# Optimization experiments

Hardware: AMD Instinct MI355X
Metric: run time of the kernel (lower is better)

The kernel has to match this reference:

```python
import jax, jax.numpy as jnp
import numpy as np

B, S, HID = 1, 2048, 2048
NH, NKV, D = 32, 8, 64
GROUPS = NH // NKV
THETA = 10000.0


def _rope_tables(seq_len, dim):
    inv_freq = 1.0 / (THETA ** (jnp.arange(0, dim, 2, dtype=jnp.float32) / dim))
    t = jnp.arange(seq_len, dtype=jnp.float32)
    freqs = jnp.outer(t, inv_freq)            # [S, D/2]
    emb = jnp.concatenate([freqs, freqs], axis=-1)  # [S, D]
    return jnp.cos(emb), jnp.sin(emb)


def _rotate_half(x):
    x1, x2 = jnp.split(x, 2, axis=-1)
    return jnp.concatenate([-x2, x1], axis=-1)


def setup_inputs() -> dict:
    key = jax.random.key(0)
    ks = jax.random.split(key, 8)
    hidden_states = jax.random.normal(ks[0], (B, S, HID), dtype=jnp.float32)
    # additive causal mask, 0 on/below diagonal, -1e9 above
    causal = jnp.tril(jnp.ones((S, S), dtype=bool))
    attention_mask = jnp.where(causal, 0.0, -1e9).astype(jnp.float32)[None, None]
    sc = 0.02
    Wq = sc * jax.random.normal(ks[1], (NH * D, HID), dtype=jnp.float32)
    bq = jnp.zeros((NH * D,), dtype=jnp.float32)
    Wk = sc * jax.random.normal(ks[2], (NKV * D, HID), dtype=jnp.float32)
    bk = jnp.zeros((NKV * D,), dtype=jnp.float32)
    Wv = sc * jax.random.normal(ks[3], (NKV * D, HID), dtype=jnp.float32)
    bv = jnp.zeros((NKV * D,), dtype=jnp.float32)
    Wo = sc * jax.random.normal(ks[4], (HID, NH * D), dtype=jnp.float32)
    return {"hidden_states": hidden_states, "attention_mask": attention_mask,
            "Wq": Wq, "bq": bq, "Wk": Wk, "bk": bk, "Wv": Wv, "bv": bv, "Wo": Wo}


def reference(hidden_states, attention_mask, Wq, bq, Wk, bk, Wv, bv, Wo):
    b, s, _ = hidden_states.shape
    q = (hidden_states @ Wq.T + bq).reshape(b, s, NH, D).transpose(0, 2, 1, 3)   # [B,NH,S,D]
    k = (hidden_states @ Wk.T + bk).reshape(b, s, NKV, D).transpose(0, 2, 1, 3)  # [B,NKV,S,D]
    v = (hidden_states @ Wv.T + bv).reshape(b, s, NKV, D).transpose(0, 2, 1, 3)
    cos, sin = _rope_tables(s, D)
    cos = cos[None, None]; sin = sin[None, None]
    q = q * cos + _rotate_half(q) * sin
    k = k * cos + _rotate_half(k) * sin
    # GQA: repeat KV heads to match query heads
    k = jnp.repeat(k, GROUPS, axis=1)  # [B,NH,S,D]
    v = jnp.repeat(v, GROUPS, axis=1)
    scores = jnp.einsum('bhqd,bhkd->bhqk', q, k) / jnp.sqrt(jnp.float32(D))
    scores = jnp.clip(scores, -50.0, 50.0)
    scores = scores + attention_mask
    probs = jax.nn.softmax(scores.astype(jnp.float32), axis=-1).astype(q.dtype)
    attn = jnp.einsum('bhqk,bhkd->bhqd', probs, v)
    attn = attn.transpose(0, 2, 1, 3).reshape(b, s, NH * D)
    return attn @ Wo.T
```

## Files before the change

kernel.cpp:

```cpp
#include <hip/hip_runtime.h>
#include <hip/hip_bf16.h>
#include <stdint.h>

typedef unsigned short u16;
typedef unsigned int u32;

#define S_LEN 2048
#define HID 2048
#define NH 32
#define NKV 8
#define HD 64
#define PIT 2080

using f32x4 = __attribute__((ext_vector_type(4))) float;
using bfrag = __attribute__((ext_vector_type(8))) short;

__device__ __forceinline__ float b2f(u16 u) {
  union { u32 i; float f; } c; c.i = ((u32)u) << 16; return c.f;
}
__device__ __forceinline__ u16 f2b(float f) {
  union { float f; u32 i; } c; c.f = f;
  u32 r = c.i + 0x7fffu + ((c.i >> 16) & 1u);
  return (u16)(r >> 16);
}
__device__ __forceinline__ uint4 cvt8(const float* __restrict__ p) {
  float4 a = *(const float4*)p;
  float4 b = *(const float4*)(p + 4);
  uint4 r;
  r.x = (u32)f2b(a.x) | ((u32)f2b(a.y) << 16);
  r.y = (u32)f2b(a.z) | ((u32)f2b(a.w) << 16);
  r.z = (u32)f2b(b.x) | ((u32)f2b(b.y) << 16);
  r.w = (u32)f2b(b.z) | ((u32)f2b(b.w) << 16);
  return r;
}

__device__ __forceinline__ void gl2lds16(const u16* g, u16* l) {
  __builtin_amdgcn_global_load_lds(
      (const __attribute__((address_space(1))) void*)g,
      (__attribute__((address_space(3))) void*)l,
      16, 0, 0);
}

#define WAITBAR(N) asm volatile("s_waitcnt vmcnt(" #N ")\ns_barrier" ::: "memory")

__global__ void conv_all(const float* __restrict__ hid, const float* __restrict__ Wq,
                         const float* __restrict__ Wk, const float* __restrict__ Wv,
                         u16* __restrict__ hidb, u16* __restrict__ Wqkvb) {
  int row = blockIdx.x;
  int col = threadIdx.x * 8;
  const float* src; u16* dst;
  if (row < 2048)      { src = hid + (size_t)row * 2048;          dst = hidb  + (size_t)row * PIT; }
  else if (row < 4096) { src = Wq + (size_t)(row - 2048) * 2048;  dst = Wqkvb + (size_t)(row - 2048) * PIT; }
  else if (row < 4608) { src = Wk + (size_t)(row - 4096) * 2048;  dst = Wqkvb + (size_t)(row - 4096 + 2048) * PIT; }
  else                 { src = Wv + (size_t)(row - 4608) * 2048;  dst = Wqkvb + (size_t)(row - 4608 + 2560) * PIT; }
  *(uint4*)(dst + col) = cvt8(src + col);
}

__global__ void conv_f2b_p(const float* __restrict__ in, u16* __restrict__ out, int n8) {
  int i = blockIdx.x * 256 + threadIdx.x;
  if (i >= n8) return;
  int row = i >> 8;
  int col = (i & 255) * 8;
  *(uint4*)(out + (size_t)row * PIT + col) = cvt8(in + (size_t)row * 2048 + col);
}

__global__ __launch_bounds__(256, 3) void gemm_qkv(
    const u16* __restrict__ A, const u16* __restrict__ B,
    const float* __restrict__ bq, const float* __restrict__ bk, const float* __restrict__ bv,
    u16* __restrict__ Qb, u16* __restrict__ Kb, u16* __restrict__ Vt)
{
  __shared__ __align__(16) u16 As[3 * 2048];
  __shared__ __align__(16) u16 Bs[3 * 4096];
  __shared__ __align__(16) u16 strip_s[4][16 * 72];

  const int tid  = threadIdx.x;
  const int m0   = blockIdx.y * 64;
  const int n0   = blockIdx.x * 128;
  const int lane = tid & 63;
  const int w    = tid >> 6;
  const int wm   = w >> 1, wn = w & 1;
  const int quad = lane >> 4, l16 = lane & 15;

  const int srow = tid >> 2;
  const int scol = (tid & 3) * 8;
  const u16* ga = A + (size_t)(m0 + srow) * PIT + scol;
  const u16* gb = B + (size_t)(n0 + srow) * PIT + scol;

#define STAGE_G(bi, k0)                                                         \
  do {                                                                          \
    gl2lds16(ga + (k0), As + (bi) * 2048 + tid * 8);                            \
    gl2lds16(gb + (k0), Bs + (bi) * 4096 + tid * 8);                            \
    gl2lds16(gb + (size_t)64 * PIT + (k0), Bs + (bi) * 4096 + 2048 + tid * 8);  \
  } while (0)

  f32x4 zero = {0.f, 0.f, 0.f, 0.f};
  f32x4 acc[2][4];
#pragma unroll
  for (int mi = 0; mi < 2; ++mi)
#pragma unroll
    for (int ni = 0; ni < 4; ++ni) acc[mi][ni] = zero;

  STAGE_G(0, 0);
  STAGE_G(1, 32);

  int cur = 0;
  for (int k = 0; k < 64; ++k) {
    if (k < 63) WAITBAR(3);
    else        WAITBAR(0);
    if (k + 2 < 64) {
      int nb = cur + 2; if (nb >= 3) nb -= 3;
      STAGE_G(nb, (k + 2) * 32);
    }
    const u16* as = As + cur * 2048;
    const u16* bs = Bs + cur * 4096;

    bfrag af[2], bf[4];
#pragma unroll
    for (int i = 0; i < 2; ++i)
      af[i] = *(const bfrag*)&as[(wm * 32 + i * 16 + l16) * 32 + quad * 8];
#pragma unroll
    for (int i = 0; i < 4; ++i)
      bf[i] = *(const bfrag*)&bs[(wn * 64 + i * 16 + l16) * 32 + quad * 8];
#pragma unroll
    for (int mi = 0; mi < 2; ++mi)
#pragma unroll
      for (int ni = 0; ni < 4; ++ni)
        acc[mi][ni] = __builtin_amdgcn_mfma_f32_16x16x32_bf16(af[mi], bf[ni], acc[mi][ni], 0, 0, 0);

    cur += 1; if (cur == 3) cur = 0;
  }
#undef STAGE_G

  u16* strip = strip_s[w];
  const int rr = lane >> 2;
  const int co = (lane & 3) * 8;

  if (n0 < 2048) {
#pragma unroll
    for (int mi = 0; mi < 2; ++mi) {
#pragma unroll
      for (int n01 = 0; n01 < 2; ++n01)
#pragma unroll
        for (int i = 0; i < 4; ++i) {
          int d  = n01 * 16 + l16;
          int c1 = n0 + wn * 64 + d;
          float x1 = acc[mi][n01][i]     + bq[c1];
          float x2 = acc[mi][n01 + 2][i] + bq[c1 + 32];
          float inv = exp2f(-(float)d * 0.41524101186092034f);
          float ang = (float)(m0 + wm * 32 + mi * 16 + quad * 4 + i) * inv;
          float cs = cosf(ang), sn = sinf(ang);
          strip[(quad * 4 + i) * 72 + d]      = f2b(x1 * cs - x2 * sn);
          strip[(quad * 4 + i) * 72 + d + 32] = f2b(x2 * cs + x1 * sn);
        }
      uint4 v0 = *(const uint4*)&strip[rr * 72 + co];
      uint4 v1 = *(const uint4*)&strip[rr * 72 + 32 + co];
      size_t gb2 = (size_t)(m0 + wm * 32 + mi * 16 + rr) * 2048 + n0 + wn * 64;
      *(uint4*)(Qb + gb2 + co)      = v0;
      *(uint4*)(Qb + gb2 + 32 + co) = v1;
    }
  } else if (n0 < 2560) {
    int cb = (n0 - 2048) + wn * 64;
#pragma unroll
    for (int mi = 0; mi < 2; ++mi) {
#pragma unroll
      for (int n01 = 0; n01 < 2; ++n01)
#pragma unroll
        for (int i = 0; i < 4; ++i) {
          int d  = n01 * 16 + l16;
          int cg = cb + d;
          float x1 = acc[mi][n01][i]     + bk[cg];
          float x2 = acc[mi][n01 + 2][i] + bk[cg + 32];
          float inv = exp2f(-(float)d * 0.41524101186092034f);
          float ang = (float)(m0 + wm * 32 + mi * 16 + quad * 4 + i) * inv;
          float cs = cosf(ang), sn = sinf(ang);
          strip[(quad * 4 + i) * 72 + d]      = f2b(x1 * cs - x2 * sn);
          strip[(quad * 4 + i) * 72 + d + 32] = f2b(x2 * cs + x1 * sn);
        }
      uint4 v0 = *(const uint4*)&strip[rr * 72 + co];
      uint4 v1 = *(const uint4*)&strip[rr * 72 + 32 + co];
      size_t gb2 = (size_t)(m0 + wm * 32 + mi * 16 + rr) * 512 + cb;
      *(uint4*)(Kb + gb2 + co)      = v0;
      *(uint4*)(Kb + gb2 + 32 + co) = v1;
    }
  } else {
    int cgb = (n0 - 2560) + wn * 64;
#pragma unroll
    for (int ni = 0; ni < 4; ++ni) {
      float bvv = bv[cgb + ni * 16 + l16];
#pragma unroll
      for (int mi = 0; mi < 2; ++mi)
#pragma unroll
        for (int i = 0; i < 4; ++i)
          strip[l16 * 72 + mi * 16 + quad * 4 + i] = f2b(acc[mi][ni][i] + bvv);
      uint4 v0 = *(const uint4*)&strip[rr * 72 + co];
      size_t gb2 = (size_t)(cgb + ni * 16 + rr) * PIT + m0 + wm * 32;
      *(uint4*)(Vt + gb2 + co) = v0;
    }
  }
}

__global__ __launch_bounds__(256, 3) void gemm_o(
    const u16* __restrict__ A, const u16* __restrict__ B, float* __restrict__ C)
{
  __shared__ __align__(16) u16 As[3 * 2048];
  __shared__ __align__(16) u16 Bs[3 * 4096];

  const int tid  = threadIdx.x;
  const int m0   = blockIdx.y * 64;
  const int n0   = blockIdx.x * 128;
  const int lane = tid & 63;
  const int w    = tid >> 6;
  const int wm   = w >> 1, wn = w & 1;
  const int quad = lane >> 4, l16 = lane & 15;

  const int srow = tid >> 2;
  const int scol = (tid & 3) * 8;
  const u16* ga = A + (size_t)(m0 + srow) * PIT + scol;
  const u16* gb = B + (size_t)(n0 + srow) * PIT + scol;

#define STAGE_G(bi, k0)                                                         \
  do {                                                                          \
    gl2lds16(ga + (k0), As + (bi) * 2048 + tid * 8);                            \
    gl2lds16(gb + (k0), Bs + (bi) * 4096 + tid * 8);                            \
    gl2lds16(gb + (size_t)64 * PIT + (k0), Bs + (bi) * 4096 + 2048 + tid * 8);  \
  } while (0)

  f32x4 zero = {0.f, 0.f, 0.f, 0.f};
  f32x4 acc[2][4];
#pragma unroll
  for (int mi = 0; mi < 2; ++mi)
#pragma unroll
    for (int ni = 0; ni < 4; ++ni) acc[mi][ni] = zero;

  STAGE_G(0, 0);
  STAGE_G(1, 32);

  int cur = 0;
  for (int k = 0; k < 64; ++k) {
    if (k < 63) WAITBAR(3);
    else        WAITBAR(0);
    if (k + 2 < 64) {
      int nb = cur + 2; if (nb >= 3) nb -= 3;
      STAGE_G(nb, (k + 2) * 32);
    }
    const u16* as = As + cur * 2048;
    const u16* bs = Bs + cur * 4096;

    bfrag af[2], bf[4];
#pragma unroll
    for (int i = 0; i < 2; ++i)
      af[i] = *(const bfrag*)&as[(wm * 32 + i * 16 + l16) * 32 + quad * 8];
#pragma unroll
    for (int i = 0; i < 4; ++i)
      bf[i] = *(const bfrag*)&bs[(wn * 64 + i * 16 + l16) * 32 + quad * 8];
#pragma unroll
    for (int mi = 0; mi < 2; ++mi)
#pragma unroll
      for (int ni = 0; ni < 4; ++ni)
        acc[mi][ni] = __builtin_amdgcn_mfma_f32_16x16x32_bf16(af[mi], bf[ni], acc[mi][ni], 0, 0, 0);

    cur += 1; if (cur == 3) cur = 0;
  }
#undef STAGE_G

#pragma unroll
  for (int ni = 0; ni < 4; ++ni) {
    int col = n0 + wn * 64 + ni * 16 + l16;
#pragma unroll
    for (int mi = 0; mi < 2; ++mi)
#pragma unroll
      for (int i = 0; i < 4; ++i) {
        int row = m0 + wm * 32 + mi * 16 + quad * 4 + i;
        C[(size_t)row * 2048 + col] = acc[mi][ni][i];
      }
  }
}

#define SM_SC 0.18033688011112042f
#define SM_UB 72.134752044448169f

__global__ __launch_bounds__(256, 2) void attn_flash6(
    const u16* __restrict__ Qb, const u16* __restrict__ Kb,
    const u16* __restrict__ Vt, u16* __restrict__ Ab)
{
  __shared__ __align__(16) u16 Ks[3][64 * 64];
  __shared__ __align__(16) u16 Vs[3][64 * 64];
  __shared__ __align__(16) u16 Ps[4][16][72];

  const int h    = blockIdx.x;
  const int p    = blockIdx.y;
  const int kvh  = h >> 2;
  const int tid  = threadIdx.x;
  const int lane = tid & 63;
  const int w    = tid >> 6;
  const int quad = lane >> 4, l16 = lane & 15;

  const int qtA = 31 - p, qtB = p;
  const int nA  = qtA + 1;

  const int c0  = w * 128 + lane;
  const int r0  = c0 >> 3,        s0 = c0 & 7;
  const int r1  = (c0 + 64) >> 3, s1 = (c0 + 64) & 7;
  const int sg0 = s0 ^ (r0 & 7);
  const int sg1 = s1 ^ (r1 & 7);
  const u16* Ksrc0 = Kb + (size_t)r0 * 512 + kvh * 64 + sg0 * 8;
  const u16* Ksrc1 = Kb + (size_t)r1 * 512 + kvh * 64 + sg1 * 8;
  const u16* Vsrc0 = Vt + (size_t)(kvh * 64 + r0) * PIT + sg0 * 8;
  const u16* Vsrc1 = Vt + (size_t)(kvh * 64 + r1) * PIT + sg1 * 8;

#define STAGEKV(buf, kb)                                                        \
  do {                                                                          \
    gl2lds16(Ksrc0 + (size_t)(kb) * 32768, &Ks[buf][0] + c0 * 8);               \
    gl2lds16(Ksrc1 + (size_t)(kb) * 32768, &Ks[buf][0] + (c0 + 64) * 8);        \
    gl2lds16(Vsrc0 + (kb) * 64,            &Vs[buf][0] + c0 * 8);               \
    gl2lds16(Vsrc1 + (kb) * 64,            &Vs[buf][0] + (c0 + 64) * 8);        \
  } while (0)

  STAGEKV(0, 0);
  STAGEKV(1, 1);

  bfrag qfA0, qfA1, qfB0, qfB1;
  {
    const u16* qa = Qb + (size_t)(qtA * 64 + w * 16 + l16) * 2048 + h * 64 + quad * 8;
    const u16* qb = Qb + (size_t)(qtB * 64 + w * 16 + l16) * 2048 + h * 64 + quad * 8;
    qfA0 = *(const bfrag*)qa;  qfA1 = *(const bfrag*)(qa + 32);
    qfB0 = *(const bfrag*)qb;  qfB1 = *(const bfrag*)(qb + 32);
  }
  bfrag q0 = qfA0, q1 = qfA1;

  f32x4 zero = {0.f, 0.f, 0.f, 0.f};
  f32x4 o_acc[4];
  float lpart[4];
#pragma unroll
  for (int nb = 0; nb < 4; ++nb) { o_acc[nb] = zero; lpart[nb] = 0.f; }

  const int swz = (l16 & 7) * 8;
  int qt = qtA;
  int cur = 0;

  for (int t = 0; t < 33; ++t) {
    if (t < 32) WAITBAR(4);
    else        WAITBAR(0);
    if (t + 2 < 33) {
      int kb2 = (t + 2 < nA) ? (t + 2) : (t + 2 - nA);
      int b3 = cur + 2; if (b3 >= 3) b3 -= 3;
      STAGEKV(b3, kb2);
    }
    if (t == nA) { q0 = qfB0; q1 = qfB1; qt = qtB; }

    const u16* ks = &Ks[cur][0];
    const u16* vs = &Vs[cur][0];

    bfrag kf0[4], kf1[4];
#pragma unroll
    for (int nb = 0; nb < 4; ++nb) {
      int row = (nb * 16 + l16) * 64;
      kf0[nb] = *(const bfrag*)&ks[row + ((quad * 8) ^ swz)];
      kf1[nb] = *(const bfrag*)&ks[row + ((32 + quad * 8) ^ swz)];
    }

    const bool diag = (t == nA - 1) || (t == 32);

    f32x4 s_acc[4];
#pragma unroll
    for (int nb = 0; nb < 4; ++nb) {
      s_acc[nb] = __builtin_amdgcn_mfma_f32_16x16x32_bf16(q0, kf0[nb], zero, 0, 0, 0);
      s_acc[nb] = __builtin_amdgcn_mfma_f32_16x16x32_bf16(q1, kf1[nb], s_acc[nb], 0, 0, 0);
    }
    if (diag) {
#pragma unroll
      for (int nb = 0; nb < 4; ++nb)
#pragma unroll
        for (int i = 0; i < 4; ++i) {
          float u = s_acc[nb][i] * SM_SC;
          u = fminf(SM_UB, fmaxf(-SM_UB, u));
          bool msk = (nb * 16 + l16 > w * 16 + quad * 4 + i);
          float pr = msk ? 0.0f : __builtin_amdgcn_exp2f(u);
          lpart[i] += pr;
          Ps[w][quad * 4 + i][nb * 16 + l16] = f2b(pr);
        }
    } else {
#pragma unroll
      for (int nb = 0; nb < 4; ++nb)
#pragma unroll
        for (int i = 0; i < 4; ++i) {
          float u = s_acc[nb][i] * SM_SC;
          u = fminf(SM_UB, fmaxf(-SM_UB, u));
          float pr = __builtin_amdgcn_exp2f(u);
          lpart[i] += pr;
          Ps[w][quad * 4 + i][nb * 16 + l16] = f2b(pr);
        }
    }

    bfrag vf0[4], vf1[4];
#pragma unroll
    for (int nb = 0; nb < 4; ++nb) {
      int row = (nb * 16 + l16) * 64;
      vf0[nb] = *(const bfrag*)&vs[row + ((quad * 8) ^ swz)];
      vf1[nb] = *(const bfrag*)&vs[row + ((32 + quad * 8) ^ swz)];
    }
    {
      bfrag pf0 = *(const bfrag*)&Ps[w][l16][quad * 8];
      bfrag pf1 = *(const bfrag*)&Ps[w][l16][32 + quad * 8];
#pragma unroll
      for (int nb = 0; nb < 4; ++nb) {
        o_acc[nb] = __builtin_amdgcn_mfma_f32_16x16x32_bf16(pf0, vf0[nb], o_acc[nb], 0, 0, 0);
        o_acc[nb] = __builtin_amdgcn_mfma_f32_16x16x32_bf16(pf1, vf1[nb], o_acc[nb], 0, 0, 0);
      }
    }

    if (diag) {
#pragma unroll
      for (int off = 1; off < 16; off <<= 1)
#pragma unroll
        for (int i = 0; i < 4; ++i)
          lpart[i] += __shfl_xor(lpart[i], off, 64);
#pragma unroll
      for (int i = 0; i < 4; ++i) {
        float inv = 1.0f / lpart[i];
        size_t rbase = (size_t)(qt * 64 + w * 16 + quad * 4 + i) * PIT + h * 64;
#pragma unroll
        for (int nb = 0; nb < 4; ++nb)
          Ab[rbase + nb * 16 + l16] = f2b(o_acc[nb][i] * inv);
      }
#pragma unroll
      for (int nb = 0; nb < 4; ++nb) { o_acc[nb] = zero; lpart[nb] = 0.f; }
    }

    cur += 1; if (cur == 3) cur = 0;
  }
}

extern "C" void kernel_launch(void* const* d_in, const int* in_sizes, int n_in,
                              void* d_out, int out_size, void* d_ws, size_t ws_size,
                              hipStream_t stream) {
  const float* hid = (const float*)d_in[0];
  const float* Wq = (const float*)d_in[2];
  const float* bq = (const float*)d_in[3];
  const float* Wk = (const float*)d_in[4];
  const float* bk = (const float*)d_in[5];
  const float* Wv = (const float*)d_in[6];
  const float* bv = (const float*)d_in[7];
  const float* Wo = (const float*)d_in[8];

  u16* hidb  = (u16*)d_ws;
  u16* Wqkvb = hidb + (size_t)2048 * PIT;
  u16* Qb    = Wqkvb + (size_t)3072 * PIT;
  u16* Kb    = Qb + 4194304;
  u16* Vt    = Kb + 1048576;
  u16* Wob   = hidb;
  u16* Ab    = Wqkvb;
  float* Ob  = (float*)d_out;

  conv_all<<<5120, 256, 0, stream>>>(hid, Wq, Wk, Wv, hidb, Wqkvb);

  gemm_qkv<<<dim3(24, 32), 256, 0, stream>>>(hidb, Wqkvb, bq, bk, bv, Qb, Kb, Vt);

  conv_f2b_p<<<2048, 256, 0, stream>>>(Wo, Wob, 524288);

  attn_flash6<<<dim3(32, 16), 256, 0, stream>>>(Qb, Kb, Vt, Ab);

  gemm_o<<<dim3(16, 32), 256, 0, stream>>>(Ab, Wob, Ob);
}
```

Measured before the change: 250.0 us.

## Enlarge GEMM block tiles to 128x128 with 64x64 per-wave subtiles

Both the QKV and output-projection GEMMs move from 64x128 to 128x128 block tiles, so each wave computes a 64x64 subtile with 16 MFMA accumulators instead of 8. This raises MFMA work per LDS fragment load and halves the number of blocks, cutting global and LDS traffic per FLOP. In exchange it uses more registers and LDS, lowers the occupancy bound from 3 to 2 blocks per CU, and leaves fewer blocks (384 and 256) to fill the CUs. The epilogues, the V-transpose store and the wait counts are updated to match.

Result: slower. 273.4 us (+9.3%).

```diff
diff --git a/kernel.cpp b/kernel.cpp
--- a/kernel.cpp
+++ b/kernel.cpp
@@ -64,39 +64,38 @@
   *(uint4*)(out + (size_t)row * PIT + col) = cvt8(in + (size_t)row * 2048 + col);
 }
 
-__global__ __launch_bounds__(256, 3) void gemm_qkv(
+__global__ __launch_bounds__(256, 2) void gemm_qkv(
     const u16* __restrict__ A, const u16* __restrict__ B,
     const float* __restrict__ bq, const float* __restrict__ bk, const float* __restrict__ bv,
     u16* __restrict__ Qb, u16* __restrict__ Kb, u16* __restrict__ Vt)
 {
-  __shared__ __align__(16) u16 As[3 * 2048];
+  __shared__ __align__(16) u16 As[3 * 4096];
   __shared__ __align__(16) u16 Bs[3 * 4096];
   __shared__ __align__(16) u16 strip_s[4][16 * 72];
 
   const int tid  = threadIdx.x;
-  const int m0   = blockIdx.y * 64;
+  const int m0   = blockIdx.y * 128;
   const int n0   = blockIdx.x * 128;
   const int lane = tid & 63;
   const int w    = tid >> 6;
   const int wm   = w >> 1, wn = w & 1;
   const int quad = lane >> 4, l16 = lane & 15;
 
-  const int srow = tid >> 2;
-  const int scol = (tid & 3) * 8;
-  const u16* ga = A + (size_t)(m0 + srow) * PIT + scol;
-  const u16* gb = B + (size_t)(n0 + srow) * PIT + scol;
+  const u16* gA = A + (size_t)(m0 + (tid >> 2)) * PIT + (tid & 3) * 8;
+  const u16* gB = B + (size_t)(n0 + (tid >> 2)) * PIT + (tid & 3) * 8;
 
 #define STAGE_G(bi, k0)                                                         \
   do {                                                                          \
-    gl2lds16(ga + (k0), As + (bi) * 2048 + tid * 8);                            \
-    gl2lds16(gb + (k0), Bs + (bi) * 4096 + tid * 8);                            \
-    gl2lds16(gb + (size_t)64 * PIT + (k0), Bs + (bi) * 4096 + 2048 + tid * 8);  \
+    gl2lds16(gA + (k0), As + (bi) * 4096 + tid * 8);                            \
+    gl2lds16(gA + (size_t)64 * PIT + (k0), As + (bi) * 4096 + 2048 + tid * 8);  \
+    gl2lds16(gB + (k0), Bs + (bi) * 4096 + tid * 8);                            \
+    gl2lds16(gB + (size_t)64 * PIT + (k0), Bs + (bi) * 4096 + 2048 + tid * 8);  \
   } while (0)
 
   f32x4 zero = {0.f, 0.f, 0.f, 0.f};
-  f32x4 acc[2][4];
-#pragma unroll
-  for (int mi = 0; mi < 2; ++mi)
+  f32x4 acc[4][4];
+#pragma unroll
+  for (int mi = 0; mi < 4; ++mi)
 #pragma unroll
     for (int ni = 0; ni < 4; ++ni) acc[mi][ni] = zero;
 
@@ -105,24 +104,24 @@
 
   int cur = 0;
   for (int k = 0; k < 64; ++k) {
-    if (k < 63) WAITBAR(3);
+    if (k < 63) WAITBAR(4);
     else        WAITBAR(0);
     if (k + 2 < 64) {
       int nb = cur + 2; if (nb >= 3) nb -= 3;
       STAGE_G(nb, (k + 2) * 32);
     }
-    const u16* as = As + cur * 2048;
-    const u16* bs = Bs + cur * 4096;
-
-    bfrag af[2], bf[4];
-#pragma unroll
-    for (int i = 0; i < 2; ++i)
-      af[i] = *(const bfrag*)&as[(wm * 32 + i * 16 + l16) * 32 + quad * 8];
+    const u16* as = As + cur * 4096 + wm * 2048;
+    const u16* bs = Bs + cur * 4096 + wn * 2048;
+
+    bfrag af[4], bf[4];
 #pragma unroll
     for (int i = 0; i < 4; ++i)
-      bf[i] = *(const bfrag*)&bs[(wn * 64 + i * 16 + l16) * 32 + quad * 8];
-#pragma unroll
-    for (int mi = 0; mi < 2; ++mi)
+      af[i] = *(const bfrag*)&as[(i * 16 + l16) * 32 + quad * 8];
+#pragma unroll
+    for (int i = 0; i < 4; ++i)
+      bf[i] = *(const bfrag*)&bs[(i * 16 + l16) * 32 + quad * 8];
+#pragma unroll
+    for (int mi = 0; mi < 4; ++mi)
 #pragma unroll
       for (int ni = 0; ni < 4; ++ni)
         acc[mi][ni] = __builtin_amdgcn_mfma_f32_16x16x32_bf16(af[mi], bf[ni], acc[mi][ni], 0, 0, 0);
@@ -132,36 +131,38 @@
 #undef STAGE_G
 
   u16* strip = strip_s[w];
-  const int rr = lane >> 2;
-  const int co = (lane & 3) * 8;
+  const int rr   = lane >> 2;
+  const int co   = (lane & 3) * 8;
+  const int mrow = m0 + wm * 64;
 
   if (n0 < 2048) {
-#pragma unroll
-    for (int mi = 0; mi < 2; ++mi) {
+    int cb = n0 + wn * 64;
+#pragma unroll
+    for (int mi = 0; mi < 4; ++mi) {
 #pragma unroll
       for (int n01 = 0; n01 < 2; ++n01)
 #pragma unroll
         for (int i = 0; i < 4; ++i) {
           int d  = n01 * 16 + l16;
-          int c1 = n0 + wn * 64 + d;
+          int c1 = cb + d;
           float x1 = acc[mi][n01][i]     + bq[c1];
           float x2 = acc[mi][n01 + 2][i] + bq[c1 + 32];
           float inv = exp2f(-(float)d * 0.41524101186092034f);
-          float ang = (float)(m0 + wm * 32 + mi * 16 + quad * 4 + i) * inv;
+          float ang = (float)(mrow + mi * 16 + quad * 4 + i) * inv;
           float cs = cosf(ang), sn = sinf(ang);
           strip[(quad * 4 + i) * 72 + d]      = f2b(x1 * cs - x2 * sn);
           strip[(quad * 4 + i) * 72 + d + 32] = f2b(x2 * cs + x1 * sn);
         }
       uint4 v0 = *(const uint4*)&strip[rr * 72 + co];
       uint4 v1 = *(const uint4*)&strip[rr * 72 + 32 + co];
-      size_t gb2 = (size_t)(m0 + wm * 32 + mi * 16 + rr) * 2048 + n0 + wn * 64;
+      size_t gb2 = (size_t)(mrow + mi * 16 + rr) * 2048 + cb;
       *(uint4*)(Qb + gb2 + co)      = v0;
       *(uint4*)(Qb + gb2 + 32 + co) = v1;
     }
   } else if (n0 < 2560) {
     int cb = (n0 - 2048) + wn * 64;
 #pragma unroll
-    for (int mi = 0; mi < 2; ++mi) {
+    for (int mi = 0; mi < 4; ++mi) {
 #pragma unroll
       for (int n01 = 0; n01 < 2; ++n01)
 #pragma unroll
@@ -171,14 +172,14 @@
           float x1 = acc[mi][n01][i]     + bk[cg];
           float x2 = acc[mi][n01 + 2][i] + bk[cg + 32];
           float inv = exp2f(-(float)d * 0.41524101186092034f);
-          float ang = (float)(m0 + wm * 32 + mi * 16 + quad * 4 + i) * inv;
+          float ang = (float)(mrow + mi * 16 + quad * 4 + i) * inv;
           float cs = cosf(ang), sn = sinf(ang);
           strip[(quad * 4 + i) * 72 + d]      = f2b(x1 * cs - x2 * sn);
           strip[(quad * 4 + i) * 72 + d + 32] = f2b(x2 * cs + x1 * sn);
         }
       uint4 v0 = *(const uint4*)&strip[rr * 72 + co];
       uint4 v1 = *(const uint4*)&strip[rr * 72 + 32 + co];
-      size_t gb2 = (size_t)(m0 + wm * 32 + mi * 16 + rr) * 512 + cb;
+      size_t gb2 = (size_t)(mrow + mi * 16 + rr) * 512 + cb;
       *(uint4*)(Kb + gb2 + co)      = v0;
       *(uint4*)(Kb + gb2 + 32 + co) = v1;
     }
@@ -188,47 +189,48 @@
     for (int ni = 0; ni < 4; ++ni) {
       float bvv = bv[cgb + ni * 16 + l16];
 #pragma unroll
-      for (int mi = 0; mi < 2; ++mi)
+      for (int mi = 0; mi < 4; ++mi)
 #pragma unroll
         for (int i = 0; i < 4; ++i)
           strip[l16 * 72 + mi * 16 + quad * 4 + i] = f2b(acc[mi][ni][i] + bvv);
       uint4 v0 = *(const uint4*)&strip[rr * 72 + co];
-      size_t gb2 = (size_t)(cgb + ni * 16 + rr) * PIT + m0 + wm * 32;
-      *(uint4*)(Vt + gb2 + co) = v0;
-    }
-  }
-}
-
-__global__ __launch_bounds__(256, 3) void gemm_o(
+      uint4 v1 = *(const uint4*)&strip[rr * 72 + 32 + co];
+      size_t gb2 = (size_t)(cgb + ni * 16 + rr) * PIT + mrow;
+      *(uint4*)(Vt + gb2 + co)      = v0;
+      *(uint4*)(Vt + gb2 + 32 + co) = v1;
+    }
+  }
+}
+
+__global__ __launch_bounds__(256, 2) void gemm_o(
     const u16* __restrict__ A, const u16* __restrict__ B, float* __restrict__ C)
 {
-  __shared__ __align__(16) u16 As[3 * 2048];
+  __shared__ __align__(16) u16 As[3 * 4096];
   __shared__ __align__(16) u16 Bs[3 * 4096];
 
   const int tid  = threadIdx.x;
-  const int m0   = blockIdx.y * 64;
+  const int m0   = blockIdx.y * 128;
   const int n0   = blockIdx.x * 128;
   const int lane = tid & 63;
   const int w    = tid >> 6;
   const int wm   = w >> 1, wn = w & 1;
   const int quad = lane >> 4, l16 = lane & 15;
 
-  const int srow = tid >> 2;
-  const int scol = (tid & 3) * 8;
-  const u16* ga = A + (size_t)(m0 + srow) * PIT + scol;
-  const u16* gb = B + (size_t)(n0 + srow) * PIT + scol;
+  const u16* gA = A + (size_t)(m0 + (tid >> 2)) * PIT + (tid & 3) * 8;
+  const u16* gB = B + (size_t)(n0 + (tid >> 2)) * PIT + (tid & 3) * 8;
 
 #define STAGE_G(bi, k0)                                                         \
   do {                                                                          \
-    gl2lds16(ga + (k0), As + (bi) * 2048 + tid * 8);                            \
-    gl2lds16(gb + (k0), Bs + (bi) * 4096 + tid * 8);                            \
-    gl2lds16(gb + (size_t)64 * PIT + (k0), Bs + (bi) * 4096 + 2048 + tid * 8);  \
+    gl2lds16(gA + (k0), As + (bi) * 4096 + tid * 8);                            \
+    gl2lds16(gA + (size_t)64 * PIT + (k0), As + (bi) * 4096 + 2048 + tid * 8);  \
+    gl2lds16(gB + (k0), Bs + (bi) * 4096 + tid * 8);                            \
+    gl2lds16(gB + (size_t)64 * PIT + (k0), Bs + (bi) * 4096 + 2048 + tid * 8);  \
   } while (0)
 
   f32x4 zero = {0.f, 0.f, 0.f, 0.f};
-  f32x4 acc[2][4];
-#pragma unroll
-  for (int mi = 0; mi < 2; ++mi)
+  f32x4 acc[4][4];
+#pragma unroll
+  for (int mi = 0; mi < 4; ++mi)
 #pragma unroll
     for (int ni = 0; ni < 4; ++ni) acc[mi][ni] = zero;
 
@@ -237,24 +239,24 @@
 
   int cur = 0;
   for (int k = 0; k < 64; ++k) {
-    if (k < 63) WAITBAR(3);
+    if (k < 63) WAITBAR(4);
     else        WAITBAR(0);
     if (k + 2 < 64) {
       int nb = cur + 2; if (nb >= 3) nb -= 3;
       STAGE_G(nb, (k + 2) * 32);
     }
-    const u16* as = As + cur * 2048;
-    const u16* bs = Bs + cur * 4096;
-
-    bfrag af[2], bf[4];
-#pragma unroll
-    for (int i = 0; i < 2; ++i)
-      af[i] = *(const bfrag*)&as[(wm * 32 + i * 16 + l16) * 32 + quad * 8];
+    const u16* as = As + cur * 4096 + wm * 2048;
+    const u16* bs = Bs + cur * 4096 + wn * 2048;
+
+    bfrag af[4], bf[4];
 #pragma unroll
     for (int i = 0; i < 4; ++i)
-      bf[i] = *(const bfrag*)&bs[(wn * 64 + i * 16 + l16) * 32 + quad * 8];
-#pragma unroll
-    for (int mi = 0; mi < 2; ++mi)
+      af[i] = *(const bfrag*)&as[(i * 16 + l16) * 32 + quad * 8];
+#pragma unroll
+    for (int i = 0; i < 4; ++i)
+      bf[i] = *(const bfrag*)&bs[(i * 16 + l16) * 32 + quad * 8];
+#pragma unroll
+    for (int mi = 0; mi < 4; ++mi)
 #pragma unroll
       for (int ni = 0; ni < 4; ++ni)
         acc[mi][ni] = __builtin_amdgcn_mfma_f32_16x16x32_bf16(af[mi], bf[ni], acc[mi][ni], 0, 0, 0);
@@ -267,10 +269,10 @@
   for (int ni = 0; ni < 4; ++ni) {
     int col = n0 + wn * 64 + ni * 16 + l16;
 #pragma unroll
-    for (int mi = 0; mi < 2; ++mi)
+    for (int mi = 0; mi < 4; ++mi)
 #pragma unroll
       for (int i = 0; i < 4; ++i) {
-        int row = m0 + wm * 32 + mi * 16 + quad * 4 + i;
+        int row = m0 + wm * 64 + mi * 16 + quad * 4 + i;
         C[(size_t)row * 2048 + col] = acc[mi][ni][i];
       }
   }
@@ -454,11 +456,11 @@
 
   conv_all<<<5120, 256, 0, stream>>>(hid, Wq, Wk, Wv, hidb, Wqkvb);
 
-  gemm_qkv<<<dim3(24, 32), 256, 0, stream>>>(hidb, Wqkvb, bq, bk, bv, Qb, Kb, Vt);
+  gemm_qkv<<<dim3(24, 16), 256, 0, stream>>>(hidb, Wqkvb, bq, bk, bv, Qb, Kb, Vt);
 
   conv_f2b_p<<<2048, 256, 0, stream>>>(Wo, Wob, 524288);
 
   attn_flash6<<<dim3(32, 16), 256, 0, stream>>>(Qb, Kb, Vt, Ab);
 
-  gemm_o<<<dim3(16, 32), 256, 0, stream>>>(Ab, Wob, Ob);
-}
+  gemm_o<<<dim3(16, 16), 256, 0, stream>>>(Ab, Wob, Ob);
+}
```
